# Performance work log

Hardware: AMD Instinct MI355X
Metric: run time of the kernel (lower is better)

Reference implementation:

```python
import jax, jax.numpy as jnp
import numpy as np

B, L, K = 2, 2048, 48
NUM_RBF = 16
NUM_POS = 16      # positional embedding dim
MAX_REL = 32      # max relative sequence offset
EDGE = 128        # edge feature dim
N_ATOMS = 5       # Ca, N, C, O, virtual Cb -> 25 atom pairs
EDGE_IN = NUM_POS + N_ATOMS * N_ATOMS * NUM_RBF  # 16 + 400 = 416


def setup_inputs() -> dict:
    key = jax.random.key(0)
    ks = jax.random.split(key, 6)
    # backbone coords (N, CA, C, O); scaled so pairwise distances span the RBF range [2, 22]
    X = jax.random.normal(ks[0], (B, L, 4, 3), dtype=jnp.float32) * 5.0
    mask = jnp.ones((B, L), dtype=jnp.float32)
    residue_idx = jnp.broadcast_to(jnp.arange(L, dtype=jnp.int32), (B, L))
    chain_labels = jnp.ones((B, L), dtype=jnp.int32)
    # learned params
    W_pos = jax.random.normal(ks[1], (2 * MAX_REL + 2, NUM_POS), dtype=jnp.float32) * 0.05
    b_pos = jnp.zeros((NUM_POS,), dtype=jnp.float32)
    W_edge = jax.random.normal(ks[2], (EDGE_IN, EDGE), dtype=jnp.float32) * 0.05  # no bias (ProteinMPNN)
    ln_gamma = jnp.ones((EDGE,), dtype=jnp.float32)
    ln_beta = jnp.zeros((EDGE,), dtype=jnp.float32)
    return {"X": X, "mask": mask, "residue_idx": residue_idx, "chain_labels": chain_labels,
            "W_pos": W_pos, "b_pos": b_pos, "W_edge": W_edge,
            "ln_gamma": ln_gamma, "ln_beta": ln_beta}


def _gather_nodes(nodes, e_idx):
    # nodes: [B, L, C], e_idx: [B, L, K] -> [B, L, K, C]
    b, l, k = e_idx.shape
    flat = e_idx.reshape(b, l * k)
    return jnp.take_along_axis(nodes, flat[..., None], axis=1).reshape(b, l, k, nodes.shape[-1])


def reference(X, mask, residue_idx, chain_labels, W_pos, b_pos, W_edge, ln_gamma, ln_beta):
    b, l = mask.shape
    k = min(K, l)
    N_at, Ca, C_at, O_at = X[:, :, 0], X[:, :, 1], X[:, :, 2], X[:, :, 3]

    # ---- kNN over Ca distances (masked) ----
    mask_2d = mask[:, :, None] * mask[:, None, :]
    dX = Ca[:, None, :, :] - Ca[:, :, None, :]            # [B, L, L, 3]
    D = mask_2d * jnp.sqrt(jnp.sum(dX * dX, -1) + 1e-6)    # [B, L, L]
    D_max = jnp.max(D, -1, keepdims=True)
    D_adjust = D + (1.0 - mask_2d) * D_max
    _, E_idx = jax.lax.top_k(-D_adjust, k)                 # k smallest distances -> [B, L, K]

    # ---- virtual Cb ----
    bb = Ca - N_at
    cc = C_at - Ca
    aa = jnp.cross(bb, cc)
    Cb = -0.58273431 * aa + 0.56802827 * bb - 0.54067466 * cc + Ca

    # ---- 25 pairwise atom-atom RBFs ----
    atoms = jnp.stack([Ca, N_at, C_at, O_at, Cb], axis=-2)            # [B, L, 5, 3]
    atoms_nb = _gather_nodes(atoms.reshape(b, l, N_ATOMS * 3), E_idx)  # [B, L, K, 15]
    atoms_nb = atoms_nb.reshape(b, l, k, N_ATOMS, 3)
    diff = atoms[:, :, None, :, None, :] - atoms_nb[:, :, :, None, :, :]  # [B, L, K, 5, 5, 3]
    Dp = jnp.sqrt(jnp.sum(diff * diff, -1) + 1e-6)                        # [B, L, K, 5, 5]
    mu = jnp.linspace(2.0, 22.0, NUM_RBF)
    sigma = (22.0 - 2.0) / NUM_RBF
    RBF_all = jnp.exp(-jnp.square((Dp[..., None] - mu) / sigma))          # [B, L, K, 5, 5, 16]
    RBF_all = RBF_all.reshape(b, l, k, N_ATOMS * N_ATOMS * NUM_RBF)       # [B, L, K, 400]

    # ---- relative positional encoding ----
    flat = E_idx.reshape(b, l * k)
    ridx_nb = jnp.take_along_axis(residue_idx, flat, axis=1).reshape(b, l, k)
    offset = residue_idx[:, :, None] - ridx_nb                            # [B, L, K]
    chain_nb = jnp.take_along_axis(chain_labels, flat, axis=1).reshape(b, l, k)
    same_chain = (chain_labels[:, :, None] == chain_nb).astype(jnp.int32)
    d = jnp.clip(offset + MAX_REL, 0, 2 * MAX_REL) * same_chain + (1 - same_chain) * (2 * MAX_REL + 1)
    d_onehot = jax.nn.one_hot(d, 2 * MAX_REL + 2, dtype=RBF_all.dtype)    # [B, L, K, 66]
    E_positional = d_onehot @ W_pos + b_pos                                # [B, L, K, 16]

    # ---- edge embedding + LayerNorm ----
    E = jnp.concatenate([E_positional, RBF_all], axis=-1) @ W_edge         # [B, L, K, 128]
    m = jnp.mean(E, -1, keepdims=True)
    v = jnp.mean(jnp.square(E - m), -1, keepdims=True)
    E = (E - m) * jax.lax.rsqrt(v + 1e-5) * ln_gamma + ln_beta
    return E, E_idx
```

## Files before the change

kernel.cpp:

```cpp
#include <hip/hip_runtime.h>
#include <hip/hip_bf16.h>
#include <stdint.h>

#define BB 2
#define LL 2048
#define KNN 48
#define MAXREL 32
#define EDGE_D 128
#define WFH_ELEMS 53248
#define EIDX_BYTES (BB*LL*KNN*4)
#define KT_PAD 65
#define PM_FRAGS (7 * KT_PAD)
#define TOT_FRAGS (2 * 3 * PM_FRAGS)

typedef unsigned long long u64;
typedef __bf16 bf16_t;
typedef bf16_t bf16x8 __attribute__((ext_vector_type(8)));
typedef float f32x4 __attribute__((ext_vector_type(4)));

union U16x8 { uint4 q; bf16x8 v; };

__device__ __forceinline__ u64 u64min(u64 a, u64 b) { return a < b ? a : b; }

__device__ __forceinline__ u64 shfl_xor_u64(u64 v, int m) {
    unsigned lo = __shfl_xor((unsigned)(v & 0xffffffffull), m);
    unsigned hi = __shfl_xor((unsigned)(v >> 32), m);
    return (((u64)hi) << 32) | lo;
}

__device__ __forceinline__ void split_hi_lo(float f, unsigned short& h, unsigned short& l) {
    unsigned bits = __float_as_uint(f);
    h = (unsigned short)(bits >> 16);
    float hf = __uint_as_float(bits & 0xffff0000u);
    float lo = f - hf;
    l = (unsigned short)(__float_as_uint(lo) >> 16);
}

__global__ __launch_bounds__(256) void prep_kernel(const float* __restrict__ W,
                                                   unsigned short* __restrict__ Wf)
{
    int tid = blockIdx.x * 256 + threadIdx.x;
    if (tid >= WFH_ELEMS) return;
    int e    = tid & 7;
    int lane = (tid >> 3) & 63;
    int nt   = (tid >> 9) & 7;
    int ktg  = tid >> 12;
    int k    = ktg * 32 + ((lane >> 4) << 3) + e;
    int col  = (nt << 4) + (lane & 15);
    float f  = W[k * 128 + col];
    unsigned short h, l;
    split_hi_lo(f, h, l);
    Wf[tid]             = h;
    Wf[tid + WFH_ELEMS] = l;
}

__global__ __launch_bounds__(256) void knn_kernel(
    const float* __restrict__ X, const float* __restrict__ mask,
    int* __restrict__ eidx_i, float* __restrict__ eidx_f)
{
    const int bi   = blockIdx.x;
    const int b    = bi >> 11;
    const int i    = bi & (LL - 1);
    const int tid  = threadIdx.x;
    const int wv   = tid >> 6;
    const int lane = tid & 63;

    __shared__ int   hist[256];
    __shared__ int   ctrl[4];
    __shared__ int   cnt;
    __shared__ u64   list[64];
    __shared__ float wshA[4], wshB[4];
    __shared__ u64   wmin[2][4];

    const float* Xb = X + (size_t)b * LL * 12;
    const float* mb = mask + (size_t)b * LL;

    const float cax = Xb[i * 12 + 3];
    const float cay = Xb[i * 12 + 4];
    const float caz = Xb[i * 12 + 5];
    const float mi  = mb[i];

    float D[8], M2[8];
    float dmax = 0.0f;

    #pragma unroll
    for (int t = 0; t < 8; t++) {
        int j = (t << 8) + tid;
        float dx = Xb[j * 12 + 3] - cax;
        float dy = Xb[j * 12 + 4] - cay;
        float dz = Xb[j * 12 + 5] - caz;
        float s  = __fadd_rn(__fadd_rn(__fmul_rn(dx, dx), __fmul_rn(dy, dy)),
                             __fmul_rn(dz, dz));
        float m2 = __fmul_rn(mi, mb[j]);
        float d  = __fmul_rn(m2, sqrtf(__fadd_rn(s, 1e-6f)));
        D[t]  = d;
        M2[t] = m2;
        dmax  = fmaxf(dmax, d);
    }

    hist[tid] = 0;
    if (tid == 0) cnt = 0;

    #pragma unroll
    for (int off = 32; off; off >>= 1) dmax = fmaxf(dmax, __shfl_xor(dmax, off));
    if (lane == 0) wshA[wv] = dmax;
    __syncthreads();
    dmax = fmaxf(fmaxf(wshA[0], wshA[1]), fmaxf(wshA[2], wshA[3]));

    u64 key[8];
    float dadj[8];
    float dmin = 3.4e38f;
    #pragma unroll
    for (int t = 0; t < 8; t++) {
        int j = (t << 8) + tid;
        float da = __fadd_rn(D[t], __fmul_rn(1.0f - M2[t], dmax));
        dadj[t] = da;
        key[t] = (((u64)__float_as_uint(da)) << 32) | (unsigned)j;
        dmin = fminf(dmin, da);
    }
    #pragma unroll
    for (int off = 32; off; off >>= 1) dmin = fminf(dmin, __shfl_xor(dmin, off));
    if (lane == 0) wshB[wv] = dmin;
    __syncthreads();
    dmin = fminf(fminf(wshB[0], wshB[1]), fminf(wshB[2], wshB[3]));

    const float range = dmax - dmin;
    const float scale = (range > 1e-35f) ? (255.0f / range) : 0.0f;

    int bin[8];
    #pragma unroll
    for (int t = 0; t < 8; t++) {
        int bb = (int)((dadj[t] - dmin) * scale);
        bin[t] = bb > 255 ? 255 : bb;
        atomicAdd(&hist[bin[t]], 1);
    }
    __syncthreads();

    if (wv == 0) {
        int h0 = hist[4 * lane], h1 = hist[4 * lane + 1];
        int h2 = hist[4 * lane + 2], h3 = hist[4 * lane + 3];
        int s = h0 + h1 + h2 + h3;
        int sc = s;
        #pragma unroll
        for (int off = 1; off < 64; off <<= 1) {
            int o = __shfl_up(sc, off);
            if (lane >= off) sc += o;
        }
        u64 ball = __ballot(sc >= KNN);
        int fl = __ffsll((unsigned long long)ball) - 1;
        if (lane == fl) {
            int cb = sc - s;
            int B, cbB, m1;
            if      (cb + h0 >= KNN)           { B = 4*lane;   cbB = cb;          m1 = cb+h0; }
            else if (cb + h0 + h1 >= KNN)      { B = 4*lane+1; cbB = cb+h0;       m1 = cb+h0+h1; }
            else if (cb + h0 + h1 + h2 >= KNN) { B = 4*lane+2; cbB = cb+h0+h1;    m1 = cb+h0+h1+h2; }
            else                               { B = 4*lane+3; cbB = cb+h0+h1+h2; m1 = cb+h0+h1+h2+h3; }
            ctrl[0] = B; ctrl[1] = cbB; ctrl[2] = m1;
        }
    }
    __syncthreads();
    const int B = ctrl[0], cbB = ctrl[1], m1 = ctrl[2];

    if (m1 <= 64) {
        #pragma unroll
        for (int t = 0; t < 8; t++) {
            if (bin[t] <= B) { int p = atomicAdd(&cnt, 1); list[p] = key[t]; }
        }
        __syncthreads();
        if (wv == 0) {
            u64 v = (lane < m1) ? list[lane] : ~0ull;
            #pragma unroll
            for (int k = 2; k <= 64; k <<= 1)
                #pragma unroll
                for (int j = k >> 1; j > 0; j >>= 1) {
                    u64 o = shfl_xor_u64(v, j);
                    bool takemin = (((lane & k) == 0) == ((lane & j) == 0));
                    u64 mn = u64min(v, o);
                    u64 mx = v ^ o ^ mn;
                    v = takemin ? mn : mx;
                }
            if (lane < KNN) {
                int j = (int)(v & 0xffffffffu);
                eidx_i[(size_t)bi * KNN + lane] = j;
                eidx_f[(size_t)bi * KNN + lane] = (float)j;
            }
        }
        return;
    }

    hist[tid] = 0;
    __syncthreads();
    const float width  = range * (1.0f / 255.0f);
    const float b_lo   = dmin + (float)B * width;
    const float scale2 = (width > 1e-35f) ? (255.0f / width) : 0.0f;
    int bin2[8];
    #pragma unroll
    for (int t = 0; t < 8; t++) {
        if (bin[t] == B) {
            int bb = (int)((dadj[t] - b_lo) * scale2);
            bb = bb < 0 ? 0 : (bb > 255 ? 255 : bb);
            bin2[t] = bb;
            atomicAdd(&hist[bb], 1);
        } else bin2[t] = 1 << 30;
    }
    __syncthreads();

    if (wv == 0) {
        const int T2 = KNN - cbB;
        int h0 = hist[4 * lane], h1 = hist[4 * lane + 1];
        int h2 = hist[4 * lane + 2], h3 = hist[4 * lane + 3];
        int s = h0 + h1 + h2 + h3;
        int sc = s;
        #pragma unroll
        for (int off = 1; off < 64; off <<= 1) {
            int o = __shfl_up(sc, off);
            if (lane >= off) sc += o;
        }
        u64 ball = __ballot(sc >= T2);
        int fl = __ffsll((unsigned long long)ball) - 1;
        if (lane == fl) {
            int cb = sc - s;
            int B2, cum;
            if      (cb + h0 >= T2)           { B2 = 4*lane;   cum = cb+h0; }
            else if (cb + h0 + h1 >= T2)      { B2 = 4*lane+1; cum = cb+h0+h1; }
            else if (cb + h0 + h1 + h2 >= T2) { B2 = 4*lane+2; cum = cb+h0+h1+h2; }
            else                              { B2 = 4*lane+3; cum = cb+h0+h1+h2+h3; }
            ctrl[2] = B2; ctrl[3] = cbB + cum;
        }
    }
    __syncthreads();
    const int B2 = ctrl[2], m2 = ctrl[3];

    if (m2 <= 64) {
        #pragma unroll
        for (int t = 0; t < 8; t++) {
            if (bin[t] < B || (bin[t] == B && bin2[t] <= B2)) {
                int p = atomicAdd(&cnt, 1); list[p] = key[t];
            }
        }
        __syncthreads();
        if (wv == 0) {
            u64 v = (lane < m2) ? list[lane] : ~0ull;
            #pragma unroll
            for (int k = 2; k <= 64; k <<= 1)
                #pragma unroll
                for (int j = k >> 1; j > 0; j >>= 1) {
                    u64 o = shfl_xor_u64(v, j);
                    bool takemin = (((lane & k) == 0) == ((lane & j) == 0));
                    u64 mn = u64min(v, o);
                    u64 mx = v ^ o ^ mn;
                    v = takemin ? mn : mx;
                }
            if (lane < KNN) {
                int j = (int)(v & 0xffffffffu);
                eidx_i[(size_t)bi * KNN + lane] = j;
                eidx_f[(size_t)bi * KNN + lane] = (float)j;
            }
        }
        return;
    }

    for (int s = 0; s < KNN; s++) {
        u64 lmin = key[0];
        #pragma unroll
        for (int t = 1; t < 8; t++) lmin = u64min(lmin, key[t]);
        #pragma unroll
        for (int off = 1; off < 64; off <<= 1) lmin = u64min(lmin, shfl_xor_u64(lmin, off));
        if (lane == 0) wmin[s & 1][wv] = lmin;
        __syncthreads();
        u64 gmin = u64min(u64min(wmin[s & 1][0], wmin[s & 1][1]),
                          u64min(wmin[s & 1][2], wmin[s & 1][3]));
        if (tid == 0) {
            int j = (int)(gmin & 0xffffffffu);
            eidx_i[(size_t)bi * KNN + s] = j;
            eidx_f[(size_t)bi * KNN + s] = (float)j;
        }
        #pragma unroll
        for (int t = 0; t < 8; t++) if (key[t] == gmin) key[t] = ~0ull;
    }
}

__global__ __launch_bounds__(512, 6) void edge_kernel(
    const float* __restrict__ X,
    const int*   __restrict__ ridx, const int* __restrict__ chain,
    const float* __restrict__ Wpos, const float* __restrict__ bpos,
    const unsigned short* __restrict__ Wf,
    const float* __restrict__ gamma, const float* __restrict__ beta,
    const int*   __restrict__ eidx_i, float* __restrict__ Eout)
{
    __shared__ __align__(16) uint4 frag[TOT_FRAGS];
    __shared__ float nbat[48][5][3];
    __shared__ float ctr[5][3];
    __shared__ int   dsel[48];
    __shared__ int   nbi[48];
    __shared__ float sumP[48][8];
    __shared__ float sqP[48][8];
    __shared__ float lnM[48], lnR[48];

    const int bi   = blockIdx.x;
    const int b    = bi >> 11;
    const int i    = bi & (LL - 1);
    const int tid  = threadIdx.x;
    const int w    = tid >> 6;
    const int lane = tid & 63;
    const float* Xb = X + (size_t)b * LL * 12;

    const unsigned short* wB = Wf + (size_t)w * 512 + (size_t)lane * 8;

    uint4 whc = *(const uint4*)(wB);
    uint4 wlc = *(const uint4*)(wB + WFH_ELEMS);
    uint4 whn, wln;

    if (tid < 48) {
        int j = eidx_i[(size_t)bi * KNN + tid];
        nbi[tid] = j;
        int off = ridx[b * LL + i] - ridx[b * LL + j];
        int sc  = (chain[b * LL + i] == chain[b * LL + j]);
        int d   = off + MAXREL;
        d = d < 0 ? 0 : (d > 2 * MAXREL ? 2 * MAXREL : d);
        dsel[tid] = sc ? d : (2 * MAXREL + 1);
    }
    if (tid >= 448 && tid < 452) {
        int a = tid - 448;
        int src = (a == 0) ? 1 : ((a == 1) ? 0 : a);
        ctr[a][0] = Xb[i * 12 + src * 3 + 0];
        ctr[a][1] = Xb[i * 12 + src * 3 + 1];
        ctr[a][2] = Xb[i * 12 + src * 3 + 2];
    }
    __syncthreads();

    if (tid < 192) {
        int e = tid >> 2, a = tid & 3;
        int src = (a == 0) ? 1 : ((a == 1) ? 0 : a);
        int j = nbi[e];
        nbat[e][a][0] = Xb[j * 12 + src * 3 + 0];
        nbat[e][a][1] = Xb[j * 12 + src * 3 + 1];
        nbat[e][a][2] = Xb[j * 12 + src * 3 + 2];
    }
    __syncthreads();

    if (tid < 48) {
        float bx = nbat[tid][0][0] - nbat[tid][1][0];
        float by = nbat[tid][0][1] - nbat[tid][1][1];
        float bz = nbat[tid][0][2] - nbat[tid][1][2];
        float cx = nbat[tid][2][0] - nbat[tid][0][0];
        float cy = nbat[tid][2][1] - nbat[tid][0][1];
        float cz = nbat[tid][2][2] - nbat[tid][0][2];
        float ax = by * cz - bz * cy;
        float ay = bz * cx - bx * cz;
        float az = bx * cy - by * cx;
        nbat[tid][4][0] = -0.58273431f * ax + 0.56802827f * bx - 0.54067466f * cx + nbat[tid][0][0];
        nbat[tid][4][1] = -0.58273431f * ay + 0.56802827f * by - 0.54067466f * cy + nbat[tid][0][1];
        nbat[tid][4][2] = -0.58273431f * az + 0.56802827f * bz - 0.54067466f * cz + nbat[tid][0][2];
    } else if (tid == 48) {
        float bx = ctr[0][0] - ctr[1][0];
        float by = ctr[0][1] - ctr[1][1];
        float bz = ctr[0][2] - ctr[1][2];
        float cx = ctr[2][0] - ctr[0][0];
        float cy = ctr[2][1] - ctr[0][1];
        float cz = ctr[2][2] - ctr[0][2];
        float ax = by * cz - bz * cy;
        float ay = bz * cx - bx * cz;
        float az = bx * cy - by * cx;
        ctr[4][0] = -0.58273431f * ax + 0.56802827f * bx - 0.54067466f * cx + ctr[0][0];
        ctr[4][1] = -0.58273431f * ay + 0.56802827f * by - 0.54067466f * cy + ctr[0][1];
        ctr[4][2] = -0.58273431f * az + 0.56802827f * bz - 0.54067466f * cz + ctr[0][2];
    }
    __syncthreads();

    unsigned short* fS = (unsigned short*)frag;

    for (int idx = tid; idx < 48 * 16; idx += 512) {
        int e = idx >> 4, p = idx & 15;
        int mt = e >> 4, r = e & 15;
        float f = Wpos[dsel[e] * 16 + p] + bpos[p];
        unsigned short h, l;
        split_hi_lo(f, h, l);
        int fr = mt * PM_FRAGS + (p >> 3) * 16 + r;
        fS[fr * 8 + (p & 7)]                     = h;
        fS[(fr + 3 * PM_FRAGS) * 8 + (p & 7)]    = l;
    }
    for (int idx = tid; idx < 48 * 16; idx += 512) {
        int e = idx >> 4, pr = idx & 15;
        if (pr < 13) {
            int mt = e >> 4, r = e & 15;
            int A = pr / 5, Bv = pr % 5;
            int klocal = 16 + pr * 16;
            int kt = klocal >> 5, qa = (klocal >> 3) & 3;
            float dx = ctr[A][0] - nbat[e][Bv][0];
            float dy = ctr[A][1] - nbat[e][Bv][1];
            float dz = ctr[A][2] - nbat[e][Bv][2];
            float d  = sqrtf(dx * dx + dy * dy + dz * dz + 1e-6f);
            uint hw[8], lw[8];
            #pragma unroll
            for (int rp = 0; rp < 8; rp++) {
                float mu0 = 2.0f + 1.3333334f * (float)(2 * rp);
                float mu1 = 2.0f + 1.3333334f * (float)(2 * rp + 1);
                float t0 = (d - mu0) * 0.8f, t1 = (d - mu1) * 0.8f;
                float v0 = __expf(-t0 * t0), v1 = __expf(-t1 * t1);
                unsigned short h0, l0, h1, l1;
                split_hi_lo(v0, h0, l0); split_hi_lo(v1, h1, l1);
                hw[rp] = (uint)h0 | ((uint)h1 << 16);
                lw[rp] = (uint)l0 | ((uint)l1 << 16);
            }
            int fr = mt * PM_FRAGS + kt * KT_PAD + qa * 16 + r;
            frag[fr]      = make_uint4(hw[0], hw[1], hw[2], hw[3]);
            frag[fr + 16] = make_uint4(hw[4], hw[5], hw[6], hw[7]);
            frag[fr + 3 * PM_FRAGS]      = make_uint4(lw[0], lw[1], lw[2], lw[3]);
            frag[fr + 3 * PM_FRAGS + 16] = make_uint4(lw[4], lw[5], lw[6], lw[7]);
        }
    }
    __syncthreads();

    const uint4* fb = frag + lane;
    f32x4 acc0 = {0.f, 0.f, 0.f, 0.f}, acc1 = acc0, acc2 = acc0;
    #pragma unroll
    for (int kt = 0; kt < 7; kt++) {
        whn = *(const uint4*)(wB + (kt + 1) * 4096);
        wln = *(const uint4*)(wB + WFH_ELEMS + (kt + 1) * 4096);
        U16x8 wh, wl, a0h, a1h, a2h, a0l, a1l, a2l;
        wh.q  = whc; wl.q = wlc;
        a0h.q = fb[0 * PM_FRAGS + kt * KT_PAD];
        a1h.q = fb[1 * PM_FRAGS + kt * KT_PAD];
        a2h.q = fb[2 * PM_FRAGS + kt * KT_PAD];
        a0l.q = fb[3 * PM_FRAGS + kt * KT_PAD];
        a1l.q = fb[4 * PM_FRAGS + kt * KT_PAD];
        a2l.q = fb[5 * PM_FRAGS + kt * KT_PAD];
        acc0 = __builtin_amdgcn_mfma_f32_16x16x32_bf16(a0h.v, wh.v, acc0, 0, 0, 0);
        acc1 = __builtin_amdgcn_mfma_f32_16x16x32_bf16(a1h.v, wh.v, acc1, 0, 0, 0);
        acc2 = __builtin_amdgcn_mfma_f32_16x16x32_bf16(a2h.v, wh.v, acc2, 0, 0, 0);
        acc0 = __builtin_amdgcn_mfma_f32_16x16x32_bf16(a0l.v, wh.v, acc0, 0, 0, 0);
        acc1 = __builtin_amdgcn_mfma_f32_16x16x32_bf16(a1l.v, wh.v, acc1, 0, 0, 0);
        acc2 = __builtin_amdgcn_mfma_f32_16x16x32_bf16(a2l.v, wh.v, acc2, 0, 0, 0);
        acc0 = __builtin_amdgcn_mfma_f32_16x16x32_bf16(a0h.v, wl.v, acc0, 0, 0, 0);
        acc1 = __builtin_amdgcn_mfma_f32_16x16x32_bf16(a1h.v, wl.v, acc1, 0, 0, 0);
        acc2 = __builtin_amdgcn_mfma_f32_16x16x32_bf16(a2h.v, wl.v, acc2, 0, 0, 0);
        whc = whn; wlc = wln;
    }
    __syncthreads();

    for (int idx = tid; idx < 48 * 16; idx += 512) {
        int e = idx >> 4, prl = idx & 15;
        if (prl < 12) {
            int mt = e >> 4, r = e & 15;
            int pr = 13 + prl;
            int A = pr / 5, Bv = pr % 5;
            int klocal = prl * 16;
            int kt = klocal >> 5, qa = (klocal >> 3) & 3;
            float dx = ctr[A][0] - nbat[e][Bv][0];
            float dy = ctr[A][1] - nbat[e][Bv][1];
            float dz = ctr[A][2] - nbat[e][Bv][2];
            float d  = sqrtf(dx * dx + dy * dy + dz * dz + 1e-6f);
            uint hw[8], lw[8];
            #pragma unroll
            for (int rp = 0; rp < 8; rp++) {
                float mu0 = 2.0f + 1.3333334f * (float)(2 * rp);
                float mu1 = 2.0f + 1.3333334f * (float)(2 * rp + 1);
                float t0 = (d - mu0) * 0.8f, t1 = (d - mu1) * 0.8f;
                float v0 = __expf(-t0 * t0), v1 = __expf(-t1 * t1);
                unsigned short h0, l0, h1, l1;
                split_hi_lo(v0, h0, l0); split_hi_lo(v1, h1, l1);
                hw[rp] = (uint)h0 | ((uint)h1 << 16);
                lw[rp] = (uint)l0 | ((uint)l1 << 16);
            }
            int fr = mt * PM_FRAGS + kt * KT_PAD + qa * 16 + r;
            frag[fr]      = make_uint4(hw[0], hw[1], hw[2], hw[3]);
            frag[fr + 16] = make_uint4(hw[4], hw[5], hw[6], hw[7]);
            frag[fr + 3 * PM_FRAGS]      = make_uint4(lw[0], lw[1], lw[2], lw[3]);
            frag[fr + 3 * PM_FRAGS + 16] = make_uint4(lw[4], lw[5], lw[6], lw[7]);
        }
    }
    __syncthreads();

    #pragma unroll
    for (int kt = 0; kt < 6; kt++) {
        if (kt < 5) {
            whn = *(const uint4*)(wB + (8 + kt) * 4096);
            wln = *(const uint4*)(wB + WFH_ELEMS + (8 + kt) * 4096);
        }
        U16x8 wh, wl, a0h, a1h, a2h, a0l, a1l, a2l;
        wh.q  = whc; wl.q = wlc;
        a0h.q = fb[0 * PM_FRAGS + kt * KT_PAD];
        a1h.q = fb[1 * PM_FRAGS + kt * KT_PAD];
        a2h.q = fb[2 * PM_FRAGS + kt * KT_PAD];
        a0l.q = fb[3 * PM_FRAGS + kt * KT_PAD];
        a1l.q = fb[4 * PM_FRAGS + kt * KT_PAD];
        a2l.q = fb[5 * PM_FRAGS + kt * KT_PAD];
        acc0 = __builtin_amdgcn_mfma_f32_16x16x32_bf16(a0h.v, wh.v, acc0, 0, 0, 0);
        acc1 = __builtin_amdgcn_mfma_f32_16x16x32_bf16(a1h.v, wh.v, acc1, 0, 0, 0);
        acc2 = __builtin_amdgcn_mfma_f32_16x16x32_bf16(a2h.v, wh.v, acc2, 0, 0, 0);
        acc0 = __builtin_amdgcn_mfma_f32_16x16x32_bf16(a0l.v, wh.v, acc0, 0, 0, 0);
        acc1 = __builtin_amdgcn_mfma_f32_16x16x32_bf16(a1l.v, wh.v, acc1, 0, 0, 0);
        acc2 = __builtin_amdgcn_mfma_f32_16x16x32_bf16(a2l.v, wh.v, acc2, 0, 0, 0);
        acc0 = __builtin_amdgcn_mfma_f32_16x16x32_bf16(a0h.v, wl.v, acc0, 0, 0, 0);
        acc1 = __builtin_amdgcn_mfma_f32_16x16x32_bf16(a1h.v, wl.v, acc1, 0, 0, 0);
        acc2 = __builtin_amdgcn_mfma_f32_16x16x32_bf16(a2h.v, wl.v, acc2, 0, 0, 0);
        whc = whn; wlc = wln;
    }

    {
        float vals[3][4] = {{acc0[0], acc0[1], acc0[2], acc0[3]},
                            {acc1[0], acc1[1], acc1[2], acc1[3]},
                            {acc2[0], acc2[1], acc2[2], acc2[3]}};
        #pragma unroll
        for (int mt = 0; mt < 3; mt++) {
            #pragma unroll
            for (int r = 0; r < 4; r++) {
                float sm = vals[mt][r], sq = sm * sm;
                #pragma unroll
                for (int off = 1; off < 16; off <<= 1) {
                    sm += __shfl_xor(sm, off);
                    sq += __shfl_xor(sq, off);
                }
                if ((lane & 15) == 0) {
                    int row = mt * 16 + ((lane >> 4) << 2) + r;
                    sumP[row][w] = sm;
                    sqP[row][w]  = sq;
                }
            }
        }
        __syncthreads();
        if (tid < 48) {
            float s = 0.f, q = 0.f;
            #pragma unroll
            for (int t = 0; t < 8; t++) { s += sumP[tid][t]; q += sqP[tid][t]; }
            float m = s * 0.0078125f;
            lnM[tid] = m;
            lnR[tid] = rsqrtf(q * 0.0078125f - m * m + 1e-5f);
        }
        __syncthreads();

        const int col = (w << 4) + (lane & 15);
        const float g  = gamma[col];
        const float bt = beta[col];
        float* Eo = Eout + (size_t)bi * KNN * EDGE_D;
        #pragma unroll
        for (int mt = 0; mt < 3; mt++) {
            #pragma unroll
            for (int r = 0; r < 4; r++) {
                int row = mt * 16 + ((lane >> 4) << 2) + r;
                Eo[(size_t)row * EDGE_D + col] =
                    (vals[mt][r] - lnM[row]) * lnR[row] * g + bt;
            }
        }
    }
}

extern "C" void kernel_launch(void* const* d_in, const int* in_sizes, int n_in,
                              void* d_out, int out_size, void* d_ws, size_t ws_size,
                              hipStream_t stream) {
    const float* X     = (const float*)d_in[0];
    const float* mask  = (const float*)d_in[1];
    const int*   ridx  = (const int*)d_in[2];
    const int*   chain = (const int*)d_in[3];
    const float* Wpos  = (const float*)d_in[4];
    const float* bpos  = (const float*)d_in[5];
    const float* Wedge = (const float*)d_in[6];
    const float* gamma = (const float*)d_in[7];
    const float* beta  = (const float*)d_in[8];

    float* out    = (float*)d_out;
    float* Eout   = out;
    float* eidx_f = out + (size_t)BB * LL * KNN * EDGE_D;
    int*   eidx_i = (int*)d_ws;
    unsigned short* Wf = (unsigned short*)((char*)d_ws + EIDX_BYTES);

    hipLaunchKernelGGL(prep_kernel, dim3((WFH_ELEMS + 255) / 256), dim3(256), 0, stream,
                       Wedge, Wf);
    hipLaunchKernelGGL(knn_kernel, dim3(BB * LL), dim3(256), 0, stream,
                       X, mask, eidx_i, eidx_f);
    hipLaunchKernelGGL(edge_kernel, dim3(BB * LL), dim3(512), 0, stream,
                       X, ridx, chain, Wpos, bpos, Wf, gamma, beta, eidx_i, Eout);
}
```

Measured before the change: 225.7 us.

## Fuse kNN and edge kernels; drop lo-split of activations to single bf16

Merges the kNN selection kernel into the edge-embedding kernel, so each 512-thread block selects its neighbours, keeps them in shared memory and goes straight into the RBF/MFMA/LayerNorm stage. This removes the global round-trip of neighbour indices and one kernel launch. The RBF and positional activations are also now rounded to a single bf16 instead of a hi/lo split, which cuts the MFMA count per k-tile from 9 to 6 and halves fragment LDS traffic, so the matmul runs as one 13-tile pass instead of two. The trade-off is lower precision on the activation side of the matmul, plus higher register and shared-memory pressure in the fused block.

```diff
diff --git a/kernel.cpp b/kernel.cpp
--- a/kernel.cpp
+++ b/kernel.cpp
@@ -8,10 +8,10 @@
 #define MAXREL 32
 #define EDGE_D 128
 #define WFH_ELEMS 53248
-#define EIDX_BYTES (BB*LL*KNN*4)
+#define NKT 13
 #define KT_PAD 65
-#define PM_FRAGS (7 * KT_PAD)
-#define TOT_FRAGS (2 * 3 * PM_FRAGS)
+#define MT_STRIDE (NKT * KT_PAD)
+#define TOT_FRAGS (3 * MT_STRIDE)
 
 typedef unsigned long long u64;
 typedef __bf16 bf16_t;
@@ -34,6 +34,11 @@
     float hf = __uint_as_float(bits & 0xffff0000u);
     float lo = f - hf;
     l = (unsigned short)(__float_as_uint(lo) >> 16);
+}
+
+__device__ __forceinline__ unsigned bf16rn(float f) {
+    unsigned u = __float_as_uint(f);
+    return (u + 0x7fffu + ((u >> 16) & 1u)) >> 16;
 }
 
 __global__ __launch_bounds__(256) void prep_kernel(const float* __restrict__ W,
@@ -54,38 +59,53 @@
     Wf[tid + WFH_ELEMS] = l;
 }
 
-__global__ __launch_bounds__(256) void knn_kernel(
+__global__ __launch_bounds__(512, 6) void fused_kernel(
     const float* __restrict__ X, const float* __restrict__ mask,
-    int* __restrict__ eidx_i, float* __restrict__ eidx_f)
+    const int*   __restrict__ ridx, const int* __restrict__ chain,
+    const float* __restrict__ Wpos, const float* __restrict__ bpos,
+    const unsigned short* __restrict__ Wf,
+    const float* __restrict__ gamma, const float* __restrict__ beta,
+    float* __restrict__ Eout, float* __restrict__ eidx_f)
 {
+    __shared__ __align__(16) uint4 frag[TOT_FRAGS];
+    __shared__ float nbat[48][5][3];
+    __shared__ float ctr[5][3];
+    __shared__ int   dsel[48];
+    __shared__ int   selj[48];
+    __shared__ float sumP[48][8];
+    __shared__ float sqP[48][8];
+    __shared__ float lnM[48], lnR[48];
+    __shared__ int   hist[256];
+    __shared__ int   ctrl[4];
+    __shared__ int   cnt;
+    __shared__ u64   list[64];
+    __shared__ float wshA[8], wshB[8];
+    __shared__ u64   wmin[2][8];
+
     const int bi   = blockIdx.x;
     const int b    = bi >> 11;
     const int i    = bi & (LL - 1);
     const int tid  = threadIdx.x;
-    const int wv   = tid >> 6;
+    const int w    = tid >> 6;
     const int lane = tid & 63;
-
-    __shared__ int   hist[256];
-    __shared__ int   ctrl[4];
-    __shared__ int   cnt;
-    __shared__ u64   list[64];
-    __shared__ float wshA[4], wshB[4];
-    __shared__ u64   wmin[2][4];
-
     const float* Xb = X + (size_t)b * LL * 12;
     const float* mb = mask + (size_t)b * LL;
+
+    const unsigned short* wB = Wf + (size_t)w * 512 + (size_t)lane * 8;
+    uint4 whc = *(const uint4*)(wB);
+    uint4 wlc = *(const uint4*)(wB + WFH_ELEMS);
+    uint4 whn, wln;
 
     const float cax = Xb[i * 12 + 3];
     const float cay = Xb[i * 12 + 4];
     const float caz = Xb[i * 12 + 5];
     const float mi  = mb[i];
 
-    float D[8], M2[8];
+    float D[4], M2[4];
     float dmax = 0.0f;
-
-    #pragma unroll
-    for (int t = 0; t < 8; t++) {
-        int j = (t << 8) + tid;
+    #pragma unroll
+    for (int t = 0; t < 4; t++) {
+        int j = (t << 9) + tid;
         float dx = Xb[j * 12 + 3] - cax;
         float dy = Xb[j * 12 + 4] - cay;
         float dz = Xb[j * 12 + 5] - caz;
@@ -98,21 +118,23 @@
         dmax  = fmaxf(dmax, d);
     }
 
-    hist[tid] = 0;
+    if (tid < 256) hist[tid] = 0;
     if (tid == 0) cnt = 0;
 
     #pragma unroll
     for (int off = 32; off; off >>= 1) dmax = fmaxf(dmax, __shfl_xor(dmax, off));
-    if (lane == 0) wshA[wv] = dmax;
-    __syncthreads();
-    dmax = fmaxf(fmaxf(wshA[0], wshA[1]), fmaxf(wshA[2], wshA[3]));
-
-    u64 key[8];
-    float dadj[8];
+    if (lane == 0) wshA[w] = dmax;
+    __syncthreads();
+    dmax = wshA[0];
+    #pragma unroll
+    for (int t = 1; t < 8; t++) dmax = fmaxf(dmax, wshA[t]);
+
+    u64 key[4];
+    float dadj[4];
     float dmin = 3.4e38f;
     #pragma unroll
-    for (int t = 0; t < 8; t++) {
-        int j = (t << 8) + tid;
+    for (int t = 0; t < 4; t++) {
+        int j = (t << 9) + tid;
         float da = __fadd_rn(D[t], __fmul_rn(1.0f - M2[t], dmax));
         dadj[t] = da;
         key[t] = (((u64)__float_as_uint(da)) << 32) | (unsigned)j;
@@ -120,23 +142,25 @@
     }
     #pragma unroll
     for (int off = 32; off; off >>= 1) dmin = fminf(dmin, __shfl_xor(dmin, off));
-    if (lane == 0) wshB[wv] = dmin;
-    __syncthreads();
-    dmin = fminf(fminf(wshB[0], wshB[1]), fminf(wshB[2], wshB[3]));
+    if (lane == 0) wshB[w] = dmin;
+    __syncthreads();
+    dmin = wshB[0];
+    #pragma unroll
+    for (int t = 1; t < 8; t++) dmin = fminf(dmin, wshB[t]);
 
     const float range = dmax - dmin;
     const float scale = (range > 1e-35f) ? (255.0f / range) : 0.0f;
 
-    int bin[8];
-    #pragma unroll
-    for (int t = 0; t < 8; t++) {
+    int bin[4];
+    #pragma unroll
+    for (int t = 0; t < 4; t++) {
         int bb = (int)((dadj[t] - dmin) * scale);
         bin[t] = bb > 255 ? 255 : bb;
         atomicAdd(&hist[bin[t]], 1);
     }
     __syncthreads();
 
-    if (wv == 0) {
+    if (w == 0) {
         int h0 = hist[4 * lane], h1 = hist[4 * lane + 1];
         int h2 = hist[4 * lane + 2], h3 = hist[4 * lane + 3];
         int s = h0 + h1 + h2 + h3;
@@ -163,11 +187,10 @@
 
     if (m1 <= 64) {
         #pragma unroll
-        for (int t = 0; t < 8; t++) {
+        for (int t = 0; t < 4; t++)
             if (bin[t] <= B) { int p = atomicAdd(&cnt, 1); list[p] = key[t]; }
-        }
-        __syncthreads();
-        if (wv == 0) {
+        __syncthreads();
+        if (w == 0) {
             u64 v = (lane < m1) ? list[lane] : ~0ull;
             #pragma unroll
             for (int k = 2; k <= 64; k <<= 1)
@@ -181,139 +204,104 @@
                 }
             if (lane < KNN) {
                 int j = (int)(v & 0xffffffffu);
-                eidx_i[(size_t)bi * KNN + lane] = j;
+                selj[lane] = j;
                 eidx_f[(size_t)bi * KNN + lane] = (float)j;
             }
         }
-        return;
-    }
-
-    hist[tid] = 0;
-    __syncthreads();
-    const float width  = range * (1.0f / 255.0f);
-    const float b_lo   = dmin + (float)B * width;
-    const float scale2 = (width > 1e-35f) ? (255.0f / width) : 0.0f;
-    int bin2[8];
-    #pragma unroll
-    for (int t = 0; t < 8; t++) {
-        if (bin[t] == B) {
-            int bb = (int)((dadj[t] - b_lo) * scale2);
-            bb = bb < 0 ? 0 : (bb > 255 ? 255 : bb);
-            bin2[t] = bb;
-            atomicAdd(&hist[bb], 1);
-        } else bin2[t] = 1 << 30;
-    }
-    __syncthreads();
-
-    if (wv == 0) {
-        const int T2 = KNN - cbB;
-        int h0 = hist[4 * lane], h1 = hist[4 * lane + 1];
-        int h2 = hist[4 * lane + 2], h3 = hist[4 * lane + 3];
-        int s = h0 + h1 + h2 + h3;
-        int sc = s;
-        #pragma unroll
-        for (int off = 1; off < 64; off <<= 1) {
-            int o = __shfl_up(sc, off);
-            if (lane >= off) sc += o;
-        }
-        u64 ball = __ballot(sc >= T2);
-        int fl = __ffsll((unsigned long long)ball) - 1;
-        if (lane == fl) {
-            int cb = sc - s;
-            int B2, cum;
-            if      (cb + h0 >= T2)           { B2 = 4*lane;   cum = cb+h0; }
-            else if (cb + h0 + h1 >= T2)      { B2 = 4*lane+1; cum = cb+h0+h1; }
-            else if (cb + h0 + h1 + h2 >= T2) { B2 = 4*lane+2; cum = cb+h0+h1+h2; }
-            else                              { B2 = 4*lane+3; cum = cb+h0+h1+h2+h3; }
-            ctrl[2] = B2; ctrl[3] = cbB + cum;
-        }
-    }
-    __syncthreads();
-    const int B2 = ctrl[2], m2 = ctrl[3];
-
-    if (m2 <= 64) {
-        #pragma unroll
-        for (int t = 0; t < 8; t++) {
-            if (bin[t] < B || (bin[t] == B && bin2[t] <= B2)) {
-                int p = atomicAdd(&cnt, 1); list[p] = key[t];
-            }
-        }
-        __syncthreads();
-        if (wv == 0) {
-            u64 v = (lane < m2) ? list[lane] : ~0ull;
-            #pragma unroll
-            for (int k = 2; k <= 64; k <<= 1)
-                #pragma unroll
-                for (int j = k >> 1; j > 0; j >>= 1) {
-                    u64 o = shfl_xor_u64(v, j);
-                    bool takemin = (((lane & k) == 0) == ((lane & j) == 0));
-                    u64 mn = u64min(v, o);
-                    u64 mx = v ^ o ^ mn;
-                    v = takemin ? mn : mx;
-                }
-            if (lane < KNN) {
-                int j = (int)(v & 0xffffffffu);
-                eidx_i[(size_t)bi * KNN + lane] = j;
-                eidx_f[(size_t)bi * KNN + lane] = (float)j;
-            }
-        }
-        return;
-    }
-
-    for (int s = 0; s < KNN; s++) {
-        u64 lmin = key[0];
-        #pragma unroll
-        for (int t = 1; t < 8; t++) lmin = u64min(lmin, key[t]);
-        #pragma unroll
-        for (int off = 1; off < 64; off <<= 1) lmin = u64min(lmin, shfl_xor_u64(lmin, off));
-        if (lane == 0) wmin[s & 1][wv] = lmin;
-        __syncthreads();
-        u64 gmin = u64min(u64min(wmin[s & 1][0], wmin[s & 1][1]),
-                          u64min(wmin[s & 1][2], wmin[s & 1][3]));
-        if (tid == 0) {
-            int j = (int)(gmin & 0xffffffffu);
-            eidx_i[(size_t)bi * KNN + s] = j;
-            eidx_f[(size_t)bi * KNN + s] = (float)j;
-        }
-        #pragma unroll
-        for (int t = 0; t < 8; t++) if (key[t] == gmin) key[t] = ~0ull;
-    }
-}
-
-__global__ __launch_bounds__(512, 6) void edge_kernel(
-    const float* __restrict__ X,
-    const int*   __restrict__ ridx, const int* __restrict__ chain,
-    const float* __restrict__ Wpos, const float* __restrict__ bpos,
-    const unsigned short* __restrict__ Wf,
-    const float* __restrict__ gamma, const float* __restrict__ beta,
-    const int*   __restrict__ eidx_i, float* __restrict__ Eout)
-{
-    __shared__ __align__(16) uint4 frag[TOT_FRAGS];
-    __shared__ float nbat[48][5][3];
-    __shared__ float ctr[5][3];
-    __shared__ int   dsel[48];
-    __shared__ int   nbi[48];
-    __shared__ float sumP[48][8];
-    __shared__ float sqP[48][8];
-    __shared__ float lnM[48], lnR[48];
-
-    const int bi   = blockIdx.x;
-    const int b    = bi >> 11;
-    const int i    = bi & (LL - 1);
-    const int tid  = threadIdx.x;
-    const int w    = tid >> 6;
-    const int lane = tid & 63;
-    const float* Xb = X + (size_t)b * LL * 12;
-
-    const unsigned short* wB = Wf + (size_t)w * 512 + (size_t)lane * 8;
-
-    uint4 whc = *(const uint4*)(wB);
-    uint4 wlc = *(const uint4*)(wB + WFH_ELEMS);
-    uint4 whn, wln;
+    } else {
+        if (tid < 256) hist[tid] = 0;
+        __syncthreads();
+        const float width  = range * (1.0f / 255.0f);
+        const float b_lo   = dmin + (float)B * width;
+        const float scale2 = (width > 1e-35f) ? (255.0f / width) : 0.0f;
+        int bin2[4];
+        #pragma unroll
+        for (int t = 0; t < 4; t++) {
+            if (bin[t] == B) {
+                int bb = (int)((dadj[t] - b_lo) * scale2);
+                bb = bb < 0 ? 0 : (bb > 255 ? 255 : bb);
+                bin2[t] = bb;
+                atomicAdd(&hist[bb], 1);
+            } else bin2[t] = 1 << 30;
+        }
+        __syncthreads();
+        if (w == 0) {
+            const int T2 = KNN - cbB;
+            int h0 = hist[4 * lane], h1 = hist[4 * lane + 1];
+            int h2 = hist[4 * lane + 2], h3 = hist[4 * lane + 3];
+            int s = h0 + h1 + h2 + h3;
+            int sc = s;
+            #pragma unroll
+            for (int off = 1; off < 64; off <<= 1) {
+                int o = __shfl_up(sc, off);
+                if (lane >= off) sc += o;
+            }
+            u64 ball = __ballot(sc >= T2);
+            int fl = __ffsll((unsigned long long)ball) - 1;
+            if (lane == fl) {
+                int cb = sc - s;
+                int B2, cum;
+                if      (cb + h0 >= T2)           { B2 = 4*lane;   cum = cb+h0; }
+                else if (cb + h0 + h1 >= T2)      { B2 = 4*lane+1; cum = cb+h0+h1; }
+                else if (cb + h0 + h1 + h2 >= T2) { B2 = 4*lane+2; cum = cb+h0+h1+h2; }
+                else                              { B2 = 4*lane+3; cum = cb+h0+h1+h2+h3; }
+                ctrl[2] = B2; ctrl[3] = cbB + cum;
+            }
+        }
+        __syncthreads();
+        const int B2 = ctrl[2], m2 = ctrl[3];
+
+        if (m2 <= 64) {
+            #pragma unroll
+            for (int t = 0; t < 4; t++)
+                if (bin[t] < B || (bin[t] == B && bin2[t] <= B2)) {
+                    int p = atomicAdd(&cnt, 1); list[p] = key[t];
+                }
+            __syncthreads();
+            if (w == 0) {
+                u64 v = (lane < m2) ? list[lane] : ~0ull;
+                #pragma unroll
+                for (int k = 2; k <= 64; k <<= 1)
+                    #pragma unroll
+                    for (int j = k >> 1; j > 0; j >>= 1) {
+                        u64 o = shfl_xor_u64(v, j);
+                        bool takemin = (((lane & k) == 0) == ((lane & j) == 0));
+                        u64 mn = u64min(v, o);
+                        u64 mx = v ^ o ^ mn;
+                        v = takemin ? mn : mx;
+                    }
+                if (lane < KNN) {
+                    int j = (int)(v & 0xffffffffu);
+                    selj[lane] = j;
+                    eidx_f[(size_t)bi * KNN + lane] = (float)j;
+                }
+            }
+        } else {
+            for (int s = 0; s < KNN; s++) {
+                u64 lmin = key[0];
+                #pragma unroll
+                for (int t = 1; t < 4; t++) lmin = u64min(lmin, key[t]);
+                #pragma unroll
+                for (int off = 1; off < 64; off <<= 1) lmin = u64min(lmin, shfl_xor_u64(lmin, off));
+                if (lane == 0) wmin[s & 1][w] = lmin;
+                __syncthreads();
+                u64 gmin = wmin[s & 1][0];
+                #pragma unroll
+                for (int t = 1; t < 8; t++) gmin = u64min(gmin, wmin[s & 1][t]);
+                if (tid == 0) {
+                    int j = (int)(gmin & 0xffffffffu);
+                    selj[s] = j;
+                    eidx_f[(size_t)bi * KNN + s] = (float)j;
+                }
+                #pragma unroll
+                for (int t = 0; t < 4; t++) if (key[t] == gmin) key[t] = ~0ull;
+            }
+        }
+    }
+    __syncthreads();
 
     if (tid < 48) {
-        int j = eidx_i[(size_t)bi * KNN + tid];
-        nbi[tid] = j;
+        int j = selj[tid];
         int off = ridx[b * LL + i] - ridx[b * LL + j];
         int sc  = (chain[b * LL + i] == chain[b * LL + j]);
         int d   = off + MAXREL;
@@ -327,12 +315,10 @@
         ctr[a][1] = Xb[i * 12 + src * 3 + 1];
         ctr[a][2] = Xb[i * 12 + src * 3 + 2];
     }
-    __syncthreads();
-
     if (tid < 192) {
         int e = tid >> 2, a = tid & 3;
         int src = (a == 0) ? 1 : ((a == 1) ? 0 : a);
-        int j = nbi[e];
+        int j = selj[e];
         nbat[e][a][0] = Xb[j * 12 + src * 3 + 0];
         nbat[e][a][1] = Xb[j * 12 + src * 3 + 1];
         nbat[e][a][2] = Xb[j * 12 + src * 3 + 2];
@@ -374,127 +360,53 @@
         int e = idx >> 4, p = idx & 15;
         int mt = e >> 4, r = e & 15;
         float f = Wpos[dsel[e] * 16 + p] + bpos[p];
-        unsigned short h, l;
-        split_hi_lo(f, h, l);
-        int fr = mt * PM_FRAGS + (p >> 3) * 16 + r;
-        fS[fr * 8 + (p & 7)]                     = h;
-        fS[(fr + 3 * PM_FRAGS) * 8 + (p & 7)]    = l;
-    }
-    for (int idx = tid; idx < 48 * 16; idx += 512) {
-        int e = idx >> 4, pr = idx & 15;
-        if (pr < 13) {
-            int mt = e >> 4, r = e & 15;
-            int A = pr / 5, Bv = pr % 5;
-            int klocal = 16 + pr * 16;
-            int kt = klocal >> 5, qa = (klocal >> 3) & 3;
-            float dx = ctr[A][0] - nbat[e][Bv][0];
-            float dy = ctr[A][1] - nbat[e][Bv][1];
-            float dz = ctr[A][2] - nbat[e][Bv][2];
-            float d  = sqrtf(dx * dx + dy * dy + dz * dz + 1e-6f);
-            uint hw[8], lw[8];
-            #pragma unroll
-            for (int rp = 0; rp < 8; rp++) {
-                float mu0 = 2.0f + 1.3333334f * (float)(2 * rp);
-                float mu1 = 2.0f + 1.3333334f * (float)(2 * rp + 1);
-                float t0 = (d - mu0) * 0.8f, t1 = (d - mu1) * 0.8f;
-                float v0 = __expf(-t0 * t0), v1 = __expf(-t1 * t1);
-                unsigned short h0, l0, h1, l1;
-                split_hi_lo(v0, h0, l0); split_hi_lo(v1, h1, l1);
-                hw[rp] = (uint)h0 | ((uint)h1 << 16);
-                lw[rp] = (uint)l0 | ((uint)l1 << 16);
-            }
-            int fr = mt * PM_FRAGS + kt * KT_PAD + qa * 16 + r;
-            frag[fr]      = make_uint4(hw[0], hw[1], hw[2], hw[3]);
-            frag[fr + 16] = make_uint4(hw[4], hw[5], hw[6], hw[7]);
-            frag[fr + 3 * PM_FRAGS]      = make_uint4(lw[0], lw[1], lw[2], lw[3]);
-            frag[fr + 3 * PM_FRAGS + 16] = make_uint4(lw[4], lw[5], lw[6], lw[7]);
-        }
+        int fr = mt * MT_STRIDE + (p >> 3) * 16 + r;
+        fS[fr * 8 + (p & 7)] = (unsigned short)bf16rn(f);
+    }
+    for (int idx = tid; idx < 48 * 25; idx += 512) {
+        int e = idx / 25, pr = idx % 25;
+        int mt = e >> 4, r = e & 15;
+        int A = pr / 5, Bv = pr % 5;
+        int klocal = 16 + pr * 16;
+        int kt = klocal >> 5, qa = (klocal >> 3) & 3;
+        float dx = ctr[A][0] - nbat[e][Bv][0];
+        float dy = ctr[A][1] - nbat[e][Bv][1];
+        float dz = ctr[A][2] - nbat[e][Bv][2];
+        float d  = sqrtf(dx * dx + dy * dy + dz * dz + 1e-6f);
+        uint hw[8];
+        #pragma unroll
+        for (int rp = 0; rp < 8; rp++) {
+            float mu0 = 2.0f + 1.3333334f * (float)(2 * rp);
+            float mu1 = 2.0f + 1.3333334f * (float)(2 * rp + 1);
+            float t0 = (d - mu0) * 0.8f, t1 = (d - mu1) * 0.8f;
+            float v0 = __expf(-t0 * t0), v1 = __expf(-t1 * t1);
+            hw[rp] = bf16rn(v0) | (bf16rn(v1) << 16);
+        }
+        int fr = mt * MT_STRIDE + kt * KT_PAD + qa * 16 + r;
+        frag[fr]      = make_uint4(hw[0], hw[1], hw[2], hw[3]);
+        frag[fr + 16] = make_uint4(hw[4], hw[5], hw[6], hw[7]);
     }
     __syncthreads();
 
     const uint4* fb = frag + lane;
     f32x4 acc0 = {0.f, 0.f, 0.f, 0.f}, acc1 = acc0, acc2 = acc0;
     #pragma unroll
-    for (int kt = 0; kt < 7; kt++) {
-        whn = *(const uint4*)(wB + (kt + 1) * 4096);
-        wln = *(const uint4*)(wB + WFH_ELEMS + (kt + 1) * 4096);
-        U16x8 wh, wl, a0h, a1h, a2h, a0l, a1l, a2l;
-        wh.q  = whc; wl.q = wlc;
-        a0h.q = fb[0 * PM_FRAGS + kt * KT_PAD];
-        a1h.q = fb[1 * PM_FRAGS + kt * KT_PAD];
-        a2h.q = fb[2 * PM_FRAGS + kt * KT_PAD];
-        a0l.q = fb[3 * PM_FRAGS + kt * KT_PAD];
-        a1l.q = fb[4 * PM_FRAGS + kt * KT_PAD];
-        a2l.q = fb[5 * PM_FRAGS + kt * KT_PAD];
-        acc0 = __builtin_amdgcn_mfma_f32_16x16x32_bf16(a0h.v, wh.v, acc0, 0, 0, 0);
-        acc1 = __builtin_amdgcn_mfma_f32_16x16x32_bf16(a1h.v, wh.v, acc1, 0, 0, 0);
-        acc2 = __builtin_amdgcn_mfma_f32_16x16x32_bf16(a2h.v, wh.v, acc2, 0, 0, 0);
-        acc0 = __builtin_amdgcn_mfma_f32_16x16x32_bf16(a0l.v, wh.v, acc0, 0, 0, 0);
-        acc1 = __builtin_amdgcn_mfma_f32_16x16x32_bf16(a1l.v, wh.v, acc1, 0, 0, 0);
-        acc2 = __builtin_amdgcn_mfma_f32_16x16x32_bf16(a2l.v, wh.v, acc2, 0, 0, 0);
-        acc0 = __builtin_amdgcn_mfma_f32_16x16x32_bf16(a0h.v, wl.v, acc0, 0, 0, 0);
-        acc1 = __builtin_amdgcn_mfma_f32_16x16x32_bf16(a1h.v, wl.v, acc1, 0, 0, 0);
-        acc2 = __builtin_amdgcn_mfma_f32_16x16x32_bf16(a2h.v, wl.v, acc2, 0, 0, 0);
-        whc = whn; wlc = wln;
-    }
-    __syncthreads();
-
-    for (int idx = tid; idx < 48 * 16; idx += 512) {
-        int e = idx >> 4, prl = idx & 15;
-        if (prl < 12) {
-            int mt = e >> 4, r = e & 15;
-            int pr = 13 + prl;
-            int A = pr / 5, Bv = pr % 5;
-            int klocal = prl * 16;
-            int kt = klocal >> 5, qa = (klocal >> 3) & 3;
-            float dx = ctr[A][0] - nbat[e][Bv][0];
-            float dy = ctr[A][1] - nbat[e][Bv][1];
-            float dz = ctr[A][2] - nbat[e][Bv][2];
-            float d  = sqrtf(dx * dx + dy * dy + dz * dz + 1e-6f);
-            uint hw[8], lw[8];
-            #pragma unroll
-            for (int rp = 0; rp < 8; rp++) {
-                float mu0 = 2.0f + 1.3333334f * (float)(2 * rp);
-                float mu1 = 2.0f + 1.3333334f * (float)(2 * rp + 1);
-                float t0 = (d - mu0) * 0.8f, t1 = (d - mu1) * 0.8f;
-                float v0 = __expf(-t0 * t0), v1 = __expf(-t1 * t1);
-                unsigned short h0, l0, h1, l1;
-                split_hi_lo(v0, h0, l0); split_hi_lo(v1, h1, l1);
-                hw[rp] = (uint)h0 | ((uint)h1 << 16);
-                lw[rp] = (uint)l0 | ((uint)l1 << 16);
-            }
-            int fr = mt * PM_FRAGS + kt * KT_PAD + qa * 16 + r;
-            frag[fr]      = make_uint4(hw[0], hw[1], hw[2], hw[3]);
-            frag[fr + 16] = make_uint4(hw[4], hw[5], hw[6], hw[7]);
-            frag[fr + 3 * PM_FRAGS]      = make_uint4(lw[0], lw[1], lw[2], lw[3]);
-            frag[fr + 3 * PM_FRAGS + 16] = make_uint4(lw[4], lw[5], lw[6], lw[7]);
-        }
-    }
-    __syncthreads();
-
-    #pragma unroll
-    for (int kt = 0; kt < 6; kt++) {
-        if (kt < 5) {
-            whn = *(const uint4*)(wB + (8 + kt) * 4096);
-            wln = *(const uint4*)(wB + WFH_ELEMS + (8 + kt) * 4096);
-        }
-        U16x8 wh, wl, a0h, a1h, a2h, a0l, a1l, a2l;
-        wh.q  = whc; wl.q = wlc;
-        a0h.q = fb[0 * PM_FRAGS + kt * KT_PAD];
-        a1h.q = fb[1 * PM_FRAGS + kt * KT_PAD];
-        a2h.q = fb[2 * PM_FRAGS + kt * KT_PAD];
-        a0l.q = fb[3 * PM_FRAGS + kt * KT_PAD];
-        a1l.q = fb[4 * PM_FRAGS + kt * KT_PAD];
-        a2l.q = fb[5 * PM_FRAGS + kt * KT_PAD];
-        acc0 = __builtin_amdgcn_mfma_f32_16x16x32_bf16(a0h.v, wh.v, acc0, 0, 0, 0);
-        acc1 = __builtin_amdgcn_mfma_f32_16x16x32_bf16(a1h.v, wh.v, acc1, 0, 0, 0);
-        acc2 = __builtin_amdgcn_mfma_f32_16x16x32_bf16(a2h.v, wh.v, acc2, 0, 0, 0);
-        acc0 = __builtin_amdgcn_mfma_f32_16x16x32_bf16(a0l.v, wh.v, acc0, 0, 0, 0);
-        acc1 = __builtin_amdgcn_mfma_f32_16x16x32_bf16(a1l.v, wh.v, acc1, 0, 0, 0);
-        acc2 = __builtin_amdgcn_mfma_f32_16x16x32_bf16(a2l.v, wh.v, acc2, 0, 0, 0);
-        acc0 = __builtin_amdgcn_mfma_f32_16x16x32_bf16(a0h.v, wl.v, acc0, 0, 0, 0);
-        acc1 = __builtin_amdgcn_mfma_f32_16x16x32_bf16(a1h.v, wl.v, acc1, 0, 0, 0);
-        acc2 = __builtin_amdgcn_mfma_f32_16x16x32_bf16(a2h.v, wl.v, acc2, 0, 0, 0);
+    for (int kt = 0; kt < NKT; kt++) {
+        if (kt < NKT - 1) {
+            whn = *(const uint4*)(wB + (kt + 1) * 4096);
+            wln = *(const uint4*)(wB + WFH_ELEMS + (kt + 1) * 4096);
+        }
+        U16x8 wh, wl, a0, a1, a2;
+        wh.q = whc; wl.q = wlc;
+        a0.q = fb[0 * MT_STRIDE + kt * KT_PAD];
+        a1.q = fb[1 * MT_STRIDE + kt * KT_PAD];
+        a2.q = fb[2 * MT_STRIDE + kt * KT_PAD];
+        acc0 = __builtin_amdgcn_mfma_f32_16x16x32_bf16(a0.v, wh.v, acc0, 0, 0, 0);
+        acc1 = __builtin_amdgcn_mfma_f32_16x16x32_bf16(a1.v, wh.v, acc1, 0, 0, 0);
+        acc2 = __builtin_amdgcn_mfma_f32_16x16x32_bf16(a2.v, wh.v, acc2, 0, 0, 0);
+        acc0 = __builtin_amdgcn_mfma_f32_16x16x32_bf16(a0.v, wl.v, acc0, 0, 0, 0);
+        acc1 = __builtin_amdgcn_mfma_f32_16x16x32_bf16(a1.v, wl.v, acc1, 0, 0, 0);
+        acc2 = __builtin_amdgcn_mfma_f32_16x16x32_bf16(a2.v, wl.v, acc2, 0, 0, 0);
         whc = whn; wlc = wln;
     }
 
@@ -562,13 +474,11 @@
     float* out    = (float*)d_out;
     float* Eout   = out;
     float* eidx_f = out + (size_t)BB * LL * KNN * EDGE_D;
-    int*   eidx_i = (int*)d_ws;
-    unsigned short* Wf = (unsigned short*)((char*)d_ws + EIDX_BYTES);
+    unsigned short* Wf = (unsigned short*)d_ws;
 
     hipLaunchKernelGGL(prep_kernel, dim3((WFH_ELEMS + 255) / 256), dim3(256), 0, stream,
                        Wedge, Wf);
-    hipLaunchKernelGGL(knn_kernel, dim3(BB * LL), dim3(256), 0, stream,
-                       X, mask, eidx_i, eidx_f);
-    hipLaunchKernelGGL(edge_kernel, dim3(BB * LL), dim3(512), 0, stream,
-                       X, ridx, chain, Wpos, bpos, Wf, gamma, beta, eidx_i, Eout);
-}
+    hipLaunchKernelGGL(fused_kernel, dim3(BB * LL), dim3(512), 0, stream,
+                       X, mask, ridx, chain, Wpos, bpos, Wf, gamma, beta,
+                       Eout, eidx_f);
+}
```

Measured after the change: 209.8 us. 1.08x faster.
